# Kernel optimization log

Measured on AMD Instinct MI355X. Metric: run time of the kernel, lower is better.

The kernel has to match this reference:

```python
import jax, jax.numpy as jnp
import numpy as np

B, S, D = 256, 512, 768
SEP_ID = 2
BOS_ID = 0
PAD_ID = 1


def setup_inputs() -> dict:
    key = jax.random.key(0)
    k_h, = jax.random.split(key, 1)
    hidden_states = jax.random.normal(k_h, (B, S, D), dtype=jnp.float32)

    rng = np.random.default_rng(0)
    ids = rng.integers(5, 64000, size=(B, S), dtype=np.int64)
    mask = np.zeros((B, S), dtype=np.int64)
    title_len = rng.integers(3, 60, size=B)
    lead_len = rng.integers(10, 300, size=B)
    for i in range(B):
        tl, ll = int(title_len[i]), int(lead_len[i])
        ids[i, 0] = BOS_ID
        ids[i, 1 + tl] = SEP_ID          # first </s>
        ids[i, 2 + tl] = SEP_ID          # second </s>
        lead_end = 3 + tl + ll           # position of third </s>
        lead_end = min(lead_end, S - 1)
        ids[i, 3 + tl:lead_end] = rng.integers(5, 64000, size=lead_end - (3 + tl))
        ids[i, lead_end] = SEP_ID        # third </s>
        ids[i, lead_end + 1:] = PAD_ID
        mask[i, :lead_end + 1] = 1
    return {
        "hidden_states": hidden_states,
        "input_ids": jnp.asarray(ids),
        "attention_mask": jnp.asarray(mask),
        "sep_token_id": SEP_ID,
    }


def reference(hidden_states, input_ids, attention_mask, sep_token_id):
    Bsz, Slen, _ = hidden_states.shape
    idx = jnp.arange(Slen)
    sep = input_ids == sep_token_id                     # [B,S] bool
    cnt = jnp.cumsum(sep.astype(jnp.int32), axis=1)     # running sep count

    def kth_sep_pos(k):
        # position of k-th sep token; Slen sentinel if absent
        return jnp.min(jnp.where(sep & (cnt == k), idx[None, :], Slen), axis=1)

    pos1, pos2, pos3 = kth_sep_pos(1), kth_sep_pos(2), kth_sep_pos(3)
    nsep = sep.sum(axis=1)
    attn_len = attention_mask.sum(axis=1).astype(jnp.int32)

    title_end = pos1                                   # title = tokens [1, title_end)
    lead_start = pos2 + 1
    lead_end = jnp.where(nsep >= 3, pos3, attn_len)    # lead = tokens [lead_start, lead_end)

    tmask = (idx[None, :] >= 1) & (idx[None, :] < title_end[:, None])
    lmask = (idx[None, :] >= lead_start[:, None]) & (idx[None, :] < lead_end[:, None])

    def masked_mean(m):
        mf = m.astype(hidden_states.dtype)
        n = mf.sum(axis=1)                             # [B]
        s = jnp.einsum('bs,bsd->bd', mf, hidden_states)
        return s / jnp.maximum(n, 1.0)[:, None], n

    tmean, tn = masked_mean(tmask)
    lmean, ln = masked_mean(lmask)

    cls = hidden_states[:, 0, :]
    valid = nsep >= 2
    title_pool = jnp.where((valid & (tn > 0))[:, None], tmean, cls)
    lead_pool = jnp.where((valid & (ln > 0))[:, None], lmean, cls)
    return title_pool, lead_pool
```

## Files before the change

kernel.cpp:

```cpp
#include <hip/hip_runtime.h>

#define BATCH 256
#define SEQ   512
#define DIM   768
#define D4    192
#define NW    8
#define NTHR  (NW * 64)
#define ZCH   3

__global__ __launch_bounds__(NTHR) void seg_pool_fused(
    const float* __restrict__ hidden,
    const int*  __restrict__ ids,
    const int*  __restrict__ amask,
    const int*  __restrict__ sep_tok,
    float* __restrict__ out)
{
    const int b    = blockIdx.x;
    const int seg  = blockIdx.y;
    const int z    = blockIdx.z;
    const int t    = threadIdx.x;
    const int w    = t >> 6;
    const int lane = t & 63;

    __shared__ unsigned long long s_msep[NW];
    __shared__ int    s_att[NW];
    __shared__ int    s_info[2];
    __shared__ float4 s_red[NW][64];

    {
        const int id = ids[b * SEQ + t];
        const int am = amask[b * SEQ + t];
        const unsigned long long m  = __ballot(id == sep_tok[0]);
        const unsigned long long ma = __ballot(am != 0);
        if (lane == 0) { s_msep[w] = m; s_att[w] = __popcll(ma); }
    }
    __syncthreads();

    if (t == 0) {
        int nsep = 0, p0 = SEQ, p1 = SEQ, p2 = SEQ, attn = 0;
        #pragma unroll
        for (int c = 0; c < NW; ++c) {
            attn += s_att[c];
            unsigned long long mm = s_msep[c];
            while (mm) {
                const int bit = __ffsll((long long)mm) - 1;
                const int pos = c * 64 + bit;
                if (nsep == 0)      p0 = pos;
                else if (nsep == 1) p1 = pos;
                else if (nsep == 2) p2 = pos;
                ++nsep;
                mm &= mm - 1;
            }
        }
        const bool valid = (nsep >= 2);
        int start, n;
        if (seg == 0) {
            start = 1;
            n = p0 - 1;
        } else {
            start = p1 + 1;
            const int lead_end = (nsep >= 3) ? p2 : attn;
            n = lead_end - start;
        }
        if (n < 0 || !valid) n = 0;
        s_info[0] = start;
        s_info[1] = n;
    }
    __syncthreads();

    const int start = s_info[0];
    const int n     = s_info[1];
    const int d4    = z * 64 + lane;

    const float4* __restrict__ h4 = (const float4*)hidden;
    const size_t base = (size_t)b * (SEQ * D4);

    const int chunk = (n + NW - 1) / NW;
    const int s0    = start + w * chunk;
    int s1          = s0 + chunk;
    const int send  = start + n;
    if (s1 > send) s1 = send;

    float4 acc = {0.f, 0.f, 0.f, 0.f};
    #pragma unroll 8
    for (int s = s0; s < s1; ++s) {
        const float4 v = h4[base + (size_t)s * D4 + d4];
        acc.x += v.x; acc.y += v.y; acc.z += v.z; acc.w += v.w;
    }
    s_red[w][lane] = acc;
    __syncthreads();

    if (t < 64) {
        float4 res;
        if (n > 0) {
            float4 a = {0.f, 0.f, 0.f, 0.f};
            #pragma unroll
            for (int c = 0; c < NW; ++c) {
                const float4 v = s_red[c][t];
                a.x += v.x; a.y += v.y; a.z += v.z; a.w += v.w;
            }
            const float fn = (float)n;
            res.x = a.x / fn; res.y = a.y / fn;
            res.z = a.z / fn; res.w = a.w / fn;
        } else {
            res = h4[base + d4];
        }
        float4* __restrict__ o4 = (float4*)out;
        o4[(size_t)seg * (BATCH * D4) + (size_t)b * D4 + d4] = res;
    }
}

extern "C" void kernel_launch(void* const* d_in, const int* in_sizes, int n_in,
                              void* d_out, int out_size, void* d_ws, size_t ws_size,
                              hipStream_t stream) {
    const float* hidden  = (const float*)d_in[0];
    const int*   ids     = (const int*)d_in[1];
    const int*   amask   = (const int*)d_in[2];
    const int*   sep_tok = (const int*)d_in[3];
    float*       out     = (float*)d_out;

    seg_pool_fused<<<dim3(BATCH, 2, ZCH), dim3(NTHR), 0, stream>>>(
        hidden, ids, amask, sep_tok, out);
}
```

Baseline: 30.72 us.

## Load attention mask only when needed and reorder grid so lead blocks run first

The attention-mask read and its ballot now happen only when a sample has fewer than three separators and the lead segment needs its length, so most blocks skip that global load. The grid is reordered so the z chunk is the y dimension and the segment is the z dimension, with the segment index flipped so the longer lead segments are scheduled first; the output index is remapped to match. The unroll factor of the sequence accumulation loop is raised from 8 to 16. The extra conditional barrier path adds some control flow, and the higher unroll may raise register pressure.

```diff
diff --git a/kernel.cpp b/kernel.cpp
--- a/kernel.cpp
+++ b/kernel.cpp
@@ -16,31 +16,28 @@
     float* __restrict__ out)
 {
     const int b    = blockIdx.x;
-    const int seg  = blockIdx.y;
-    const int z    = blockIdx.z;
+    const int z    = blockIdx.y;
+    const int seg  = blockIdx.z;
     const int t    = threadIdx.x;
     const int w    = t >> 6;
     const int lane = t & 63;
 
     __shared__ unsigned long long s_msep[NW];
     __shared__ int    s_att[NW];
-    __shared__ int    s_info[2];
+    __shared__ int    s_info[3];
     __shared__ float4 s_red[NW][64];
 
     {
         const int id = ids[b * SEQ + t];
-        const int am = amask[b * SEQ + t];
-        const unsigned long long m  = __ballot(id == sep_tok[0]);
-        const unsigned long long ma = __ballot(am != 0);
-        if (lane == 0) { s_msep[w] = m; s_att[w] = __popcll(ma); }
+        const unsigned long long m = __ballot(id == sep_tok[0]);
+        if (lane == 0) s_msep[w] = m;
     }
     __syncthreads();
 
     if (t == 0) {
-        int nsep = 0, p0 = SEQ, p1 = SEQ, p2 = SEQ, attn = 0;
+        int nsep = 0, p0 = SEQ, p1 = SEQ, p2 = SEQ;
         #pragma unroll
         for (int c = 0; c < NW; ++c) {
-            attn += s_att[c];
             unsigned long long mm = s_msep[c];
             while (mm) {
                 const int bit = __ffsll((long long)mm) - 1;
@@ -53,20 +50,37 @@
             }
         }
         const bool valid = (nsep >= 2);
-        int start, n;
-        if (seg == 0) {
-            start = 1;
-            n = p0 - 1;
+        if (seg == 1) {
+            int n = p0 - 1;
+            if (n < 0 || !valid) n = 0;
+            s_info[0] = 1; s_info[1] = n; s_info[2] = 0;
+        } else if (nsep >= 3) {
+            int n = p2 - (p1 + 1);
+            if (n < 0) n = 0;
+            s_info[0] = p1 + 1; s_info[1] = n; s_info[2] = 0;
         } else {
-            start = p1 + 1;
-            const int lead_end = (nsep >= 3) ? p2 : attn;
-            n = lead_end - start;
+            s_info[0] = p1 + 1;
+            s_info[1] = valid ? -1 : 0;
+            s_info[2] = valid ? 1 : 0;
         }
-        if (n < 0 || !valid) n = 0;
-        s_info[0] = start;
-        s_info[1] = n;
     }
     __syncthreads();
+
+    if (s_info[2]) {
+        const int am = amask[b * SEQ + t];
+        const unsigned long long ma = __ballot(am != 0);
+        if (lane == 0) s_att[w] = __popcll(ma);
+        __syncthreads();
+        if (t == 0) {
+            int attn = 0;
+            #pragma unroll
+            for (int c = 0; c < NW; ++c) attn += s_att[c];
+            int n = attn - s_info[0];
+            if (n < 0) n = 0;
+            s_info[1] = n;
+        }
+        __syncthreads();
+    }
 
     const int start = s_info[0];
     const int n     = s_info[1];
@@ -82,7 +96,7 @@
     if (s1 > send) s1 = send;
 
     float4 acc = {0.f, 0.f, 0.f, 0.f};
-    #pragma unroll 8
+    #pragma unroll 16
     for (int s = s0; s < s1; ++s) {
         const float4 v = h4[base + (size_t)s * D4 + d4];
         acc.x += v.x; acc.y += v.y; acc.z += v.z; acc.w += v.w;
@@ -105,8 +119,9 @@
         } else {
             res = h4[base + d4];
         }
+        const int seg_out = 1 - seg;
         float4* __restrict__ o4 = (float4*)out;
-        o4[(size_t)seg * (BATCH * D4) + (size_t)b * D4 + d4] = res;
+        o4[(size_t)seg_out * (BATCH * D4) + (size_t)b * D4 + d4] = res;
     }
 }
 
@@ -119,6 +134,6 @@
     const int*   sep_tok = (const int*)d_in[3];
     float*       out     = (float*)d_out;
 
-    seg_pool_fused<<<dim3(BATCH, 2, ZCH), dim3(NTHR), 0, stream>>>(
+    seg_pool_fused<<<dim3(BATCH, ZCH, 2), dim3(NTHR), 0, stream>>>(
         hidden, ids, amask, sep_tok, out);
 }
```

Measured after the change: 30.39 us. Within noise of the previous version (-1.1%).
